# Optimization experiments

Hardware: AMD Instinct MI355X
Metric: run time of the kernel (lower is better)

## Reference

```python
import jax, jax.numpy as jnp
import numpy as np

WINDOW = 14

def _make_rel_index(ws):
    coords = np.stack(np.meshgrid(np.arange(ws), np.arange(ws), indexing='ij'))  # [2,ws,ws]
    flat = coords.reshape(2, -1)
    rel = flat[:, :, None] - flat[:, None, :]            # [2,N,N]
    rel = rel.transpose(1, 2, 0).copy()
    rel[:, :, 0] += ws - 1
    rel[:, :, 1] += ws - 1
    rel[:, :, 0] *= 2 * ws - 1
    return rel.sum(-1).astype(np.int32)                  # [N,N]

def setup_inputs() -> dict:
    key = jax.random.key(0)
    ks = jax.random.split(key, 7)
    B, N, C, H = 256, WINDOW * WINDOW, 768, 12
    s = 0.02
    return {
        'x': jax.random.normal(ks[0], (B, N, C), jnp.float32),
        'qkv_w': jax.random.normal(ks[1], (3 * C, C), jnp.float32) * s,
        'q_bias': jnp.zeros((C,), jnp.float32),
        'v_bias': jnp.zeros((C,), jnp.float32),
        'rpb_table': jax.random.normal(ks[2], ((2 * WINDOW - 1) ** 2, H), jnp.float32) * s,
        'proj_w': jax.random.normal(ks[3], (C, C), jnp.float32) * s,
        'proj_b': jnp.zeros((C,), jnp.float32),
        'rel_index': jnp.asarray(_make_rel_index(WINDOW)),
        'num_heads': H,
    }

def reference(x, qkv_w, q_bias, v_bias, rpb_table, proj_w, proj_b, rel_index, num_heads):
    B, N, C = x.shape
    H = num_heads
    hd = C // H
    scale = hd ** -0.5
    qkv_bias = jnp.concatenate([q_bias, jnp.zeros_like(v_bias), v_bias])
    qkv = x @ qkv_w.T + qkv_bias                          # [B,N,3C]
    qkv = qkv.reshape(B, N, 3, H, hd).transpose(2, 0, 3, 1, 4)  # [3,B,H,N,hd]
    q, k, v = qkv[0] * scale, qkv[1], qkv[2]
    attn = jnp.einsum('bhnd,bhmd->bhnm', q, k)            # [B,H,N,N]
    rpb = rpb_table[rel_index.reshape(-1)].reshape(N, N, H).transpose(2, 0, 1)  # [H,N,N]
    attn = jax.nn.softmax(attn + rpb, axis=-1)
    out = jnp.einsum('bhnm,bhmd->bhnd', attn, v)          # [B,H,N,hd]
    out = out.transpose(0, 2, 1, 3).reshape(B, N, C)
    return out @ proj_w.T + proj_b
```

## Files before the change

### kernel.cpp

```cpp
#include <hip/hip_runtime.h>
#include <hip/hip_fp16.h>

typedef _Float16 f16;
typedef __attribute__((ext_vector_type(8))) _Float16 f16x8;
typedef __attribute__((ext_vector_type(4))) float f32x4;

#define MFMA16 __builtin_amdgcn_mfma_f32_16x16x32_f16

__device__ __forceinline__ void gload16(const f16* g, char* l) {
  __builtin_amdgcn_global_load_lds(
      (const __attribute__((address_space(1))) void*)g,
      (__attribute__((address_space(3))) void*)l, 16, 0, 0);
}

__global__ __launch_bounds__(256) void cvt_k(const float* __restrict__ in,
                                             f16* __restrict__ out, int n8) {
  int i = blockIdx.x * 256 + threadIdx.x;
  const int stride = gridDim.x * 256;
  for (; i < n8; i += stride) {
    const float4* p = (const float4*)(in + (size_t)i * 8);
    float4 a = p[0], b = p[1];
    f16x8 h;
    h[0] = (f16)a.x; h[1] = (f16)a.y; h[2] = (f16)a.z; h[3] = (f16)a.w;
    h[4] = (f16)b.x; h[5] = (f16)b.y; h[6] = (f16)b.z; h[7] = (f16)b.w;
    *(f16x8*)(out + (size_t)i * 8) = h;
  }
}

__global__ __launch_bounds__(256) void rpb_build_k(const float* __restrict__ tab,
                                                   const int* __restrict__ rel,
                                                   f16* __restrict__ out) {
  int i = blockIdx.x * 256 + threadIdx.x;
  if (i >= 196 * 196) return;
  int idx = rel[i];
#pragma unroll
  for (int h = 0; h < 12; ++h)
    out[h * (196 * 196) + i] = (f16)tab[idx * 12 + h];
}

template <int MODE>
__global__ __launch_bounds__(256) void gemm_k(
    const f16* __restrict__ A, const f16* __restrict__ W,
    const float* __restrict__ bias_a, const float* __restrict__ bias_b,
    f16* __restrict__ q_out, f16* __restrict__ k_out, f16* __restrict__ vT_out,
    float* __restrict__ f_out) {
  constexpr int NTIL = (MODE == 0) ? 18 : 6;
  constexpr int CPX = (MODE == 0) ? 882 : 294;
  constexpr int KT = 12;

  __shared__ char lds[32768];
  char* Asb = lds;
  char* Bsb = lds + 16384;

  const int tid = threadIdx.x;
  const int lbid = (blockIdx.x & 7) * CPX + (blockIdx.x >> 3);
  const int bcol = lbid % NTIL, brow = lbid / NTIL;
  const int lane = tid & 63, wid = tid >> 6;
  const int wrow = wid >> 1, wcol = wid & 1;
  const int l15 = lane & 15, g4 = lane >> 4;

  const int srow = tid >> 3;
  const int scol = ((tid & 7) ^ (srow & 7)) * 8;
  const f16* pA = A + (size_t)(brow * 128 + srow) * 768 + scol;
  const f16* pB = W + (size_t)(bcol * 128 + srow) * 768 + scol;
  char* ldsA = Asb + wid * 1024;
  char* ldsB = Bsb + wid * 1024;

  const f32x4 zero4 = {0.f, 0.f, 0.f, 0.f};
  f32x4 acc[4][4];
#pragma unroll
  for (int i = 0; i < 4; ++i)
#pragma unroll
    for (int j = 0; j < 4; ++j) acc[i][j] = zero4;

  const int swz = (l15 & 7);
  for (int kt = 0; kt < KT; ++kt) {
#pragma unroll
    for (int i = 0; i < 4; ++i) {
      gload16(pA + (size_t)i * 32 * 768 + kt * 64, ldsA + i * 4096);
      gload16(pB + (size_t)i * 32 * 768 + kt * 64, ldsB + i * 4096);
    }
    __syncthreads();
#pragma unroll
    for (int ks = 0; ks < 2; ++ks) {
      f16x8 af[4], bf[4];
#pragma unroll
      for (int f = 0; f < 4; ++f) {
        const int ra = wrow * 64 + f * 16 + l15;
        const int rb = wcol * 64 + f * 16 + l15;
        const int c = ((ks * 4 + g4) ^ swz) * 16;
        af[f] = *(const f16x8*)(Asb + ra * 128 + c);
        bf[f] = *(const f16x8*)(Bsb + rb * 128 + c);
      }
#pragma unroll
      for (int i = 0; i < 4; ++i)
#pragma unroll
        for (int j = 0; j < 4; ++j)
          acc[i][j] = MFMA16(af[i], bf[j], acc[i][j], 0, 0, 0);
    }
    __syncthreads();
  }

  if constexpr (MODE == 0) {
    const int s = bcol / 6;
#pragma unroll
    for (int i = 0; i < 4; ++i) {
#pragma unroll
      for (int r = 0; r < 4; ++r) {
        const int row = brow * 128 + wrow * 64 + i * 16 + g4 * 4 + r;
        const int bI = row / 196;
        const int nI = row - bI * 196;
#pragma unroll
        for (int j = 0; j < 4; ++j) {
          const int col = bcol * 128 + wcol * 64 + j * 16 + l15;
          const int rem = col - s * 768;
          const int hh = rem >> 6, dd = rem & 63;
          float v = acc[i][j][r];
          if (s == 0) {
            v = (v + bias_a[rem]) * 0.125f;
            q_out[(((size_t)bI * 12 + hh) * 196 + nI) * 64 + dd] = (f16)v;
          } else if (s == 1) {
            k_out[(((size_t)bI * 12 + hh) * 196 + nI) * 64 + dd] = (f16)v;
          } else {
            v += bias_b[rem];
            vT_out[(((size_t)bI * 12 + hh) * 64 + dd) * 224 + nI] = (f16)v;
          }
        }
      }
    }
  } else {
#pragma unroll
    for (int i = 0; i < 4; ++i) {
#pragma unroll
      for (int r = 0; r < 4; ++r) {
        const int row = brow * 128 + wrow * 64 + i * 16 + g4 * 4 + r;
        float* orow = f_out + (size_t)row * 768;
#pragma unroll
        for (int j = 0; j < 4; ++j) {
          const int col = bcol * 128 + wcol * 64 + j * 16 + l15;
          orow[col] = acc[i][j][r] + bias_a[col];
        }
      }
    }
  }
}

__global__ __launch_bounds__(256) void attn_k(const f16* __restrict__ qg,
                                              const f16* __restrict__ kg,
                                              const f16* __restrict__ vTg,
                                              const f16* __restrict__ rpb,
                                              f16* __restrict__ og) {
  extern __shared__ char smem[];
  f16x8* Klds = (f16x8*)smem;
  f16x8* Vlds = (f16x8*)(smem + 26624);
  f16x8* Plds = (f16x8*)(smem + 59392);

  const int tid = threadIdx.x;
  const int bh = blockIdx.x;
  const int b = bh / 12, h = bh - b * 12;
  const int lane = tid & 63, wid = tid >> 6;
  const int l15 = lane & 15, g4 = lane >> 4;

  f16x8 z8;
#pragma unroll
  for (int j = 0; j < 8; ++j) z8[j] = (f16)0.f;

  const f16* kgb = kg + (size_t)bh * (196 * 64);
  for (int c = tid; c < 196 * 8; c += 256) {
    int m = c >> 3, dc = c & 7;
    Klds[m * 8 + (dc ^ (m & 7))] = *(const f16x8*)(kgb + m * 64 + dc * 8);
  }
  const f16* vgb = vTg + (size_t)bh * (64 * 224);
  for (int c = tid; c < 64 * 32; c += 256) {
    int d = c >> 5, mc = c & 31;
    f16x8 v;
    if (mc < 24) {
      v = *(const f16x8*)(vgb + d * 224 + mc * 8);
    } else if (mc == 24) {
      v = *(const f16x8*)(vgb + d * 224 + mc * 8);
#pragma unroll
      for (int j = 4; j < 8; ++j) v[j] = (f16)0.f;
    } else {
      v = z8;
    }
    Vlds[d * 32 + (mc ^ (d & 7))] = v;
  }
  f16x8* Pw = Plds + wid * (16 * 32);
  if (g4 < 2) {
    int n = l15;
    Pw[n * 32 + ((26 + g4) ^ (n & 7))] = z8;
  }
  __syncthreads();

  const f16* qgb = qg + (size_t)bh * (196 * 64);
  const f16* rpbh = rpb + (size_t)h * (196 * 196);

  for (int rt = wid; rt < 13; rt += 4) {
    const int n0 = rt * 16;
    f16x8 qf0 = *(const f16x8*)(qgb + (n0 + l15) * 64 + g4 * 8);
    f16x8 qf1 = *(const f16x8*)(qgb + (n0 + l15) * 64 + 32 + g4 * 8);

    float rv[13][4];
#pragma unroll
    for (int mt = 0; mt < 13; ++mt) {
      const int m = mt * 16 + l15;
      const int mcl = (m < 196) ? m : 195;
#pragma unroll
      for (int r = 0; r < 4; ++r) {
        const int n = n0 + g4 * 4 + r;
        const int ncl = (n < 196) ? n : 195;
        rv[mt][r] = (float)rpbh[ncl * 196 + mcl];
      }
    }

    const f32x4 zero4 = {0.f, 0.f, 0.f, 0.f};
    f32x4 s[13];
#pragma unroll
    for (int mt = 0; mt < 13; ++mt) {
      const int m = mt * 16 + l15;
      f16x8 k0 = Klds[m * 8 + ((g4) ^ (m & 7))];
      f16x8 k1 = Klds[m * 8 + ((4 + g4) ^ (m & 7))];
      s[mt] = MFMA16(qf0, k0, zero4, 0, 0, 0);
      s[mt] = MFMA16(qf1, k1, s[mt], 0, 0, 0);
    }

    float mx[4] = {-3e38f, -3e38f, -3e38f, -3e38f};
#pragma unroll
    for (int mt = 0; mt < 13; ++mt) {
      const int m = mt * 16 + l15;
#pragma unroll
      for (int r = 0; r < 4; ++r) {
        const int n = n0 + g4 * 4 + r;
        float v = (m < 196 && n < 196) ? s[mt][r] + rv[mt][r] : -1e30f;
        s[mt][r] = v;
        mx[r] = fmaxf(mx[r], v);
      }
    }
#pragma unroll
    for (int r = 0; r < 4; ++r) {
      mx[r] = fmaxf(mx[r], __shfl_xor(mx[r], 1));
      mx[r] = fmaxf(mx[r], __shfl_xor(mx[r], 2));
      mx[r] = fmaxf(mx[r], __shfl_xor(mx[r], 4));
      mx[r] = fmaxf(mx[r], __shfl_xor(mx[r], 8));
    }
    float sm[4] = {0.f, 0.f, 0.f, 0.f};
#pragma unroll
    for (int mt = 0; mt < 13; ++mt)
#pragma unroll
      for (int r = 0; r < 4; ++r) {
        float p = __expf(s[mt][r] - mx[r]);
        s[mt][r] = p;
        sm[r] += p;
      }
#pragma unroll
    for (int r = 0; r < 4; ++r) {
      sm[r] += __shfl_xor(sm[r], 1);
      sm[r] += __shfl_xor(sm[r], 2);
      sm[r] += __shfl_xor(sm[r], 4);
      sm[r] += __shfl_xor(sm[r], 8);
    }
    float rinv[4];
#pragma unroll
    for (int r = 0; r < 4; ++r) rinv[r] = 1.f / sm[r];

#pragma unroll
    for (int mt = 0; mt < 13; ++mt) {
      const int m = mt * 16 + l15;
#pragma unroll
      for (int r = 0; r < 4; ++r) {
        const int n = g4 * 4 + r;
        f16* dst = (f16*)Pw + n * 256 + (((m >> 3) ^ (n & 7)) << 3) + (m & 7);
        *dst = (f16)s[mt][r];
      }
    }

    f32x4 o[4];
#pragma unroll
    for (int dt = 0; dt < 4; ++dt) o[dt] = zero4;
#pragma unroll
    for (int ks = 0; ks < 7; ++ks) {
      f16x8 pa = Pw[l15 * 32 + ((ks * 4 + g4) ^ (l15 & 7))];
#pragma unroll
      for (int dt = 0; dt < 4; ++dt) {
        const int d = dt * 16 + l15;
        f16x8 vf = Vlds[d * 32 + ((ks * 4 + g4) ^ (d & 7))];
        o[dt] = MFMA16(pa, vf, o[dt], 0, 0, 0);
      }
    }

#pragma unroll
    for (int r = 0; r < 4; ++r) {
      const int n = n0 + g4 * 4 + r;
      if (n < 196) {
        f16* orow = og + ((size_t)b * 196 + n) * 768 + h * 64;
#pragma unroll
        for (int dt = 0; dt < 4; ++dt)
          orow[dt * 16 + l15] = (f16)(o[dt][r] * rinv[r]);
      }
    }
  }
}

extern "C" void kernel_launch(void* const* d_in, const int* in_sizes, int n_in,
                              void* d_out, int out_size, void* d_ws, size_t ws_size,
                              hipStream_t stream) {
  const float* x = (const float*)d_in[0];
  const float* qkv_w = (const float*)d_in[1];
  const float* q_bias = (const float*)d_in[2];
  const float* v_bias = (const float*)d_in[3];
  const float* rpb_tab = (const float*)d_in[4];
  const float* proj_w = (const float*)d_in[5];
  const float* proj_b = (const float*)d_in[6];
  const int* rel = (const int*)d_in[7];
  float* out = (float*)d_out;

  const size_t SZ_Q = 77070336;
  const size_t SZ_K = 77070336;
  const size_t SZ_VT = 88080384;
  const size_t SZ_AO = 77070336;
  const size_t SZ_RP = 921984;
  const size_t SZ_WQ = 3538944;
  const size_t SZ_WP = 1179648;
  if (ws_size < SZ_Q + SZ_K + SZ_VT + SZ_AO + SZ_RP + SZ_WQ + SZ_WP) return;

  char* w = (char*)d_ws;
  f16* q_ = (f16*)w;
  f16* k_ = (f16*)(w + SZ_Q);
  f16* vT_ = (f16*)(w + SZ_Q + SZ_K);
  f16* ao_ = (f16*)(w + SZ_Q + SZ_K + SZ_VT);
  f16* rp_ = (f16*)(w + SZ_Q + SZ_K + SZ_VT + SZ_AO);
  f16* whq_ = (f16*)(w + SZ_Q + SZ_K + SZ_VT + SZ_AO + SZ_RP);
  f16* whp_ = (f16*)(w + SZ_Q + SZ_K + SZ_VT + SZ_AO + SZ_RP + SZ_WQ);
  f16* xh_ = ao_;

  (void)hipFuncSetAttribute((const void*)attn_k,
                            hipFuncAttributeMaxDynamicSharedMemorySize, 92160);

  cvt_k<<<2048, 256, 0, stream>>>(x, xh_, 50176 * 768 / 8);
  cvt_k<<<864, 256, 0, stream>>>(qkv_w, whq_, 2304 * 768 / 8);
  cvt_k<<<288, 256, 0, stream>>>(proj_w, whp_, 768 * 768 / 8);
  rpb_build_k<<<(196 * 196 + 255) / 256, 256, 0, stream>>>(rpb_tab, rel, rp_);

  gemm_k<0><<<392 * 18, 256, 0, stream>>>(xh_, whq_, q_bias, v_bias,
                                          q_, k_, vT_, nullptr);
  attn_k<<<3072, 256, 92160, stream>>>(q_, k_, vT_, rp_, ao_);
  gemm_k<1><<<392 * 6, 256, 0, stream>>>(ao_, whp_, proj_b, nullptr,
                                         nullptr, nullptr, nullptr, out);
}
```

Measured before the change: 822.5 us.

## Rewrite GEMM as 256x256 tile, 8-wave, double-buffered pipelined kernel

Replaces the 128x128, 4-wave, single-buffered GEMM with a 256x256 tile computed by 8 waves. Operand tiles are double-buffered in 128KB of dynamic LDS, and the next k-step's global-to-LDS loads are interleaved with four MFMA quadrants using explicit waitcnt, barriers and setprio. It also changes the XCD-aware block remapping to handle a workgroup count that does not divide evenly by 8. The aim is to hide load latency and raise data reuse per tile. In exchange, occupancy drops to one workgroup per CU, register pressure rises, and the QKV and proj GEMMs now launch fewer workgroups, with possible tail effects.

```diff
diff --git a/kernel.cpp b/kernel.cpp
--- a/kernel.cpp
+++ b/kernel.cpp
@@ -6,6 +6,10 @@
 typedef __attribute__((ext_vector_type(4))) float f32x4;
 
 #define MFMA16 __builtin_amdgcn_mfma_f32_16x16x32_f16
+#define BAR() __builtin_amdgcn_s_barrier()
+#define VMCNT(n) asm volatile("s_waitcnt vmcnt(" #n ")" ::: "memory")
+#define LGKM(n) asm volatile("s_waitcnt lgkmcnt(" #n ")" ::: "memory")
+#define SCHEDB() __builtin_amdgcn_sched_barrier(0)
 
 __device__ __forceinline__ void gload16(const f16* g, char* l) {
   __builtin_amdgcn_global_load_lds(
@@ -39,83 +43,135 @@
 }
 
 template <int MODE>
-__global__ __launch_bounds__(256) void gemm_k(
+__global__ __launch_bounds__(512) void gemm_k(
     const f16* __restrict__ A, const f16* __restrict__ W,
     const float* __restrict__ bias_a, const float* __restrict__ bias_b,
     f16* __restrict__ q_out, f16* __restrict__ k_out, f16* __restrict__ vT_out,
     float* __restrict__ f_out) {
-  constexpr int NTIL = (MODE == 0) ? 18 : 6;
-  constexpr int CPX = (MODE == 0) ? 882 : 294;
+  constexpr int NTIL = (MODE == 0) ? 9 : 3;
+  constexpr int NWG = (MODE == 0) ? 1764 : 588;
+  constexpr int QX = NWG / 8, RX = NWG % 8;
   constexpr int KT = 12;
 
-  __shared__ char lds[32768];
-  char* Asb = lds;
-  char* Bsb = lds + 16384;
+  extern __shared__ char lds[];
 
   const int tid = threadIdx.x;
-  const int lbid = (blockIdx.x & 7) * CPX + (blockIdx.x >> 3);
-  const int bcol = lbid % NTIL, brow = lbid / NTIL;
   const int lane = tid & 63, wid = tid >> 6;
-  const int wrow = wid >> 1, wcol = wid & 1;
+  const int xcd = blockIdx.x & 7, bix = blockIdx.x >> 3;
+  const int lbid =
+      (xcd < RX ? xcd * (QX + 1) : RX * (QX + 1) + (xcd - RX) * QX) + bix;
+  const int brow = lbid / NTIL, bcol = lbid % NTIL;
+  const int wr = wid >> 2, wc = wid & 3;
   const int l15 = lane & 15, g4 = lane >> 4;
 
-  const int srow = tid >> 3;
-  const int scol = ((tid & 7) ^ (srow & 7)) * 8;
-  const f16* pA = A + (size_t)(brow * 128 + srow) * 768 + scol;
-  const f16* pB = W + (size_t)(bcol * 128 + srow) * 768 + scol;
-  char* ldsA = Asb + wid * 1024;
-  char* ldsB = Bsb + wid * 1024;
+  const int sr = wid * 8 + (lane >> 3);
+  const int scw = ((lane & 7) ^ (lane >> 3)) * 8;
+  const f16* pAt = A + (size_t)(brow * 256 + sr) * 768 + scw;
+  const f16* pBt = W + (size_t)(bcol * 256 + sr) * 768 + scw;
+  char* ldsW = lds + wid * 1024;
+
+  auto stA = [&](int kt, int hf, int buf) {
+#pragma unroll
+    for (int i = 0; i < 2; ++i)
+      gload16(pAt + (size_t)(hf * 128 + i * 64) * 768 + kt * 64,
+              ldsW + buf * 65536 + hf * 16384 + i * 8192);
+  };
+  auto stB = [&](int kt, int hf, int buf) {
+#pragma unroll
+    for (int i = 0; i < 2; ++i)
+      gload16(pBt + (size_t)(hf * 128 + i * 64) * 768 + kt * 64,
+              ldsW + buf * 65536 + 32768 + hf * 16384 + i * 8192);
+  };
+
+  f16x8 af[2][4][2], bf[2][2][2];
+  const int aswz = l15 & 7;
+  const char* ldsAl = lds + (size_t)(wr * 128 + l15) * 128;
+  const char* ldsBl = lds + 32768 + (size_t)(wc * 64 + l15) * 128;
+
+  auto rdA = [&](int q, int buf) {
+#pragma unroll
+    for (int mf = 0; mf < 4; ++mf)
+#pragma unroll
+      for (int ks = 0; ks < 2; ++ks)
+        af[q][mf][ks] = *(const f16x8*)(ldsAl + buf * 65536 +
+                                        (q * 64 + mf * 16) * 128 +
+                                        ((ks * 4 + g4) ^ aswz) * 16);
+  };
+  auto rdB = [&](int r, int buf) {
+#pragma unroll
+    for (int nf = 0; nf < 2; ++nf)
+#pragma unroll
+      for (int ks = 0; ks < 2; ++ks)
+        bf[r][nf][ks] = *(const f16x8*)(ldsBl + buf * 65536 +
+                                        (r * 32 + nf * 16) * 128 +
+                                        ((ks * 4 + g4) ^ aswz) * 16);
+  };
 
   const f32x4 zero4 = {0.f, 0.f, 0.f, 0.f};
-  f32x4 acc[4][4];
-#pragma unroll
-  for (int i = 0; i < 4; ++i)
+  f32x4 acc[8][4];
+#pragma unroll
+  for (int i = 0; i < 8; ++i)
 #pragma unroll
     for (int j = 0; j < 4; ++j) acc[i][j] = zero4;
 
-  const int swz = (l15 & 7);
-  for (int kt = 0; kt < KT; ++kt) {
-#pragma unroll
-    for (int i = 0; i < 4; ++i) {
-      gload16(pA + (size_t)i * 32 * 768 + kt * 64, ldsA + i * 4096);
-      gload16(pB + (size_t)i * 32 * 768 + kt * 64, ldsB + i * 4096);
-    }
-    __syncthreads();
-#pragma unroll
-    for (int ks = 0; ks < 2; ++ks) {
-      f16x8 af[4], bf[4];
-#pragma unroll
-      for (int f = 0; f < 4; ++f) {
-        const int ra = wrow * 64 + f * 16 + l15;
-        const int rb = wcol * 64 + f * 16 + l15;
-        const int c = ((ks * 4 + g4) ^ swz) * 16;
-        af[f] = *(const f16x8*)(Asb + ra * 128 + c);
-        bf[f] = *(const f16x8*)(Bsb + rb * 128 + c);
-      }
-#pragma unroll
-      for (int i = 0; i < 4; ++i)
-#pragma unroll
-        for (int j = 0; j < 4; ++j)
-          acc[i][j] = MFMA16(af[i], bf[j], acc[i][j], 0, 0, 0);
-    }
-    __syncthreads();
-  }
-
-  if constexpr (MODE == 0) {
-    const int s = bcol / 6;
-#pragma unroll
-    for (int i = 0; i < 4; ++i) {
-#pragma unroll
-      for (int r = 0; r < 4; ++r) {
-        const int row = brow * 128 + wrow * 64 + i * 16 + g4 * 4 + r;
-        const int bI = row / 196;
-        const int nI = row - bI * 196;
-#pragma unroll
-        for (int j = 0; j < 4; ++j) {
-          const int col = bcol * 128 + wcol * 64 + j * 16 + l15;
+  auto mm = [&](int q, int r) {
+#pragma unroll
+    for (int ks = 0; ks < 2; ++ks)
+#pragma unroll
+      for (int mf = 0; mf < 4; ++mf)
+#pragma unroll
+        for (int nf = 0; nf < 2; ++nf)
+          acc[q * 4 + mf][r * 2 + nf] =
+              MFMA16(af[q][mf][ks], bf[r][nf][ks], acc[q * 4 + mf][r * 2 + nf],
+                     0, 0, 0);
+  };
+
+  stA(0, 0, 0); stA(0, 1, 0); stB(0, 0, 0); stB(0, 1, 0);
+  stA(1, 0, 1); stA(1, 1, 1);
+  VMCNT(4);
+  BAR();
+
+  for (int t = 0; t < KT; ++t) {
+    const int cur = t & 1, nxt = cur ^ 1;
+    rdA(0, cur); rdB(0, cur);
+    if (t + 1 < KT) stB(t + 1, 0, nxt);
+    LGKM(8);
+    BAR(); LGKM(0); SCHEDB();
+    __builtin_amdgcn_s_setprio(1); mm(0, 0); __builtin_amdgcn_s_setprio(0);
+    BAR();
+    rdA(1, cur);
+    if (t + 1 < KT) stB(t + 1, 1, nxt);
+    BAR(); LGKM(0); SCHEDB();
+    __builtin_amdgcn_s_setprio(1); mm(1, 0); __builtin_amdgcn_s_setprio(0);
+    BAR();
+    rdB(1, cur);
+    if (t + 2 < KT) stA(t + 2, 0, cur);
+    BAR(); LGKM(0); SCHEDB();
+    __builtin_amdgcn_s_setprio(1); mm(0, 1); __builtin_amdgcn_s_setprio(0);
+    BAR();
+    if (t + 2 < KT) stA(t + 2, 1, cur);
+    if (t < KT - 2) { VMCNT(4); } else if (t == KT - 2) { VMCNT(0); }
+    BAR(); SCHEDB();
+    __builtin_amdgcn_s_setprio(1); mm(1, 1); __builtin_amdgcn_s_setprio(0);
+    BAR();
+  }
+
+#pragma unroll
+  for (int mf = 0; mf < 8; ++mf) {
+    const int rowo = wr * 128 + (mf >> 2) * 64 + (mf & 3) * 16 + g4 * 4;
+#pragma unroll
+    for (int rr = 0; rr < 4; ++rr) {
+      const int grow = brow * 256 + rowo + rr;
+      if constexpr (MODE == 0) {
+        const int bI = grow / 196;
+        const int nI = grow - bI * 196;
+#pragma unroll
+        for (int nf = 0; nf < 4; ++nf) {
+          const int col = bcol * 256 + wc * 64 + (nf >> 1) * 32 + (nf & 1) * 16 + l15;
+          const int s = bcol / 3;
           const int rem = col - s * 768;
           const int hh = rem >> 6, dd = rem & 63;
-          float v = acc[i][j][r];
+          float v = acc[mf][nf][rr];
           if (s == 0) {
             v = (v + bias_a[rem]) * 0.125f;
             q_out[(((size_t)bI * 12 + hh) * 196 + nI) * 64 + dd] = (f16)v;
@@ -126,19 +182,12 @@
             vT_out[(((size_t)bI * 12 + hh) * 64 + dd) * 224 + nI] = (f16)v;
           }
         }
-      }
-    }
-  } else {
-#pragma unroll
-    for (int i = 0; i < 4; ++i) {
-#pragma unroll
-      for (int r = 0; r < 4; ++r) {
-        const int row = brow * 128 + wrow * 64 + i * 16 + g4 * 4 + r;
-        float* orow = f_out + (size_t)row * 768;
-#pragma unroll
-        for (int j = 0; j < 4; ++j) {
-          const int col = bcol * 128 + wcol * 64 + j * 16 + l15;
-          orow[col] = acc[i][j][r] + bias_a[col];
+      } else {
+        float* orow = f_out + (size_t)grow * 768;
+#pragma unroll
+        for (int nf = 0; nf < 4; ++nf) {
+          const int col = bcol * 256 + wc * 64 + (nf >> 1) * 32 + (nf & 1) * 16 + l15;
+          orow[col] = acc[mf][nf][rr] + bias_a[col];
         }
       }
     }
@@ -335,15 +384,19 @@
 
   (void)hipFuncSetAttribute((const void*)attn_k,
                             hipFuncAttributeMaxDynamicSharedMemorySize, 92160);
+  (void)hipFuncSetAttribute((const void*)gemm_k<0>,
+                            hipFuncAttributeMaxDynamicSharedMemorySize, 131072);
+  (void)hipFuncSetAttribute((const void*)gemm_k<1>,
+                            hipFuncAttributeMaxDynamicSharedMemorySize, 131072);
 
   cvt_k<<<2048, 256, 0, stream>>>(x, xh_, 50176 * 768 / 8);
   cvt_k<<<864, 256, 0, stream>>>(qkv_w, whq_, 2304 * 768 / 8);
   cvt_k<<<288, 256, 0, stream>>>(proj_w, whp_, 768 * 768 / 8);
   rpb_build_k<<<(196 * 196 + 255) / 256, 256, 0, stream>>>(rpb_tab, rel, rp_);
 
-  gemm_k<0><<<392 * 18, 256, 0, stream>>>(xh_, whq_, q_bias, v_bias,
-                                          q_, k_, vT_, nullptr);
+  gemm_k<0><<<1764, 512, 131072, stream>>>(xh_, whq_, q_bias, v_bias,
+                                           q_, k_, vT_, nullptr);
   attn_k<<<3072, 256, 92160, stream>>>(q_, k_, vT_, rp_, ao_);
-  gemm_k<1><<<392 * 6, 256, 0, stream>>>(ao_, whp_, proj_b, nullptr,
-                                         nullptr, nullptr, nullptr, out);
-}
+  gemm_k<1><<<588, 512, 131072, stream>>>(ao_, whp_, proj_b, nullptr,
+                                          nullptr, nullptr, nullptr, out);
+}
```

Measured after the change: 778.3 us. -5.4%, faster.
